# Kernel tuning notes

Hardware: AMD Instinct MI355X
Metric: run time of the kernel (lower is better)

The kernel has to match this reference:

```python
import jax, jax.numpy as jnp
import numpy as np


def setup_inputs() -> dict:
    key = jax.random.key(0)
    k1, k2, k3, k4, k5 = jax.random.split(key, 5)
    B, C, H, W = 8, 512, 64, 64
    mid = C // 8
    x = jax.random.normal(k1, (B, C, H, W), dtype=jnp.float32)
    # 1x1 convs (no bias) are just channel-mixing matrices
    Wb = jax.random.normal(k2, (mid, C), dtype=jnp.float32) * (1.0 / np.sqrt(C))
    Wc = jax.random.normal(k3, (mid, C), dtype=jnp.float32) * (1.0 / np.sqrt(C))
    Wd = jax.random.normal(k4, (C, C), dtype=jnp.float32) * (1.0 / np.sqrt(C))
    gamma = jax.random.normal(k5, (1,), dtype=jnp.float32)
    return {"x": x, "Wb": Wb, "Wc": Wc, "Wd": Wd, "gamma": gamma}


def reference(x, Wb, Wc, Wd, gamma):
    B, C, H, W = x.shape
    N = H * W
    xf = x.reshape(B, C, N)                          # (B, C, N)
    b = jnp.einsum('mc,bcn->bnm', Wb, xf)            # queries  (B, N, mid)
    c = jnp.einsum('mc,bcn->bmn', Wc, xf)            # keys     (B, mid, N)
    d = jnp.einsum('oc,bcn->bno', Wd, xf)            # values   (B, N, C)
    # unscaled scores, softmax over keys (last dim), as in the source
    attn = jax.nn.softmax(jnp.einsum('bnm,bmk->bnk', b, c), axis=-1)  # (B, N, N)
    out = jnp.einsum('bnk,bko->bno', attn, d)        # (B, N, C)
    out = out.transpose(0, 2, 1).reshape(B, C, H, W)
    return gamma * out + x
```

## Files before the change

kernel.cpp:

```cpp
#include <hip/hip_runtime.h>

typedef unsigned short u16;
typedef _Float16 f16x8 __attribute__((ext_vector_type(8)));
typedef short bf16x8 __attribute__((ext_vector_type(8)));
typedef float f32x16 __attribute__((ext_vector_type(16)));
typedef unsigned int u32x4 __attribute__((ext_vector_type(4)));
typedef unsigned int u32x2 __attribute__((ext_vector_type(2)));

#define LOG2E 1.44269504088896340736f

static __device__ __forceinline__ u16 f2h(float f){
  union { _Float16 h; u16 u; } v; v.h = (_Float16)f; return v.u;
}
static __device__ __forceinline__ u16 f2bf(float f){
  union { float f; unsigned u; } v; v.f = f;
  return (u16)((v.u + 0x7fffu + ((v.u >> 16) & 1u)) >> 16);
}
static __device__ __forceinline__ unsigned pk2bf(float lo, float hi){
  unsigned r; asm("v_cvt_pk_bf16_f32 %0, %1, %2" : "=v"(r) : "v"(lo), "v"(hi)); return r;
}
static __device__ __forceinline__ float ex2(float x){
#if __has_builtin(__builtin_amdgcn_exp2f)
  return __builtin_amdgcn_exp2f(x);
#else
  return exp2f(x);
#endif
}
#define PSWAP(a, b) asm("v_permlane32_swap_b32 %0, %1" : "+v"(a), "+v"(b))

__global__ __launch_bounds__(256) void k_tr(const float* __restrict__ x, u16* __restrict__ xt){
  int bx = blockIdx.x;
  int nb = bx & 63, cb = (bx >> 6) & 7, b = bx >> 9;
  __shared__ u16 lt[64 * 68];
  int t = threadIdx.x;
  int cl = t >> 4, n0 = (t & 15) * 4;
  const float* xp = x + ((size_t)(b * 512 + cb * 64)) * 4096 + nb * 64;
#pragma unroll
  for (int i = 0; i < 4; ++i) {
    int c = cl + i * 16;
    float4 v = *(const float4*)(xp + (size_t)c * 4096 + n0);
    u16* d = &lt[c * 68 + n0];
    d[0] = f2h(v.x); d[1] = f2h(v.y); d[2] = f2h(v.z); d[3] = f2h(v.w);
  }
  __syncthreads();
  u16* xo = xt + ((size_t)(b * 4096 + nb * 64)) * 512 + cb * 64;
#pragma unroll
  for (int i = 0; i < 2; ++i) {
    int s = t + i * 256;
    int n = s >> 3, ch = s & 7;
    u32x4 o;
#pragma unroll
    for (int j = 0; j < 4; ++j) {
      u16 a = lt[(ch * 8 + 2 * j) * 68 + n];
      u16 bb = lt[(ch * 8 + 2 * j + 1) * 68 + n];
      o[j] = (unsigned)a | ((unsigned)bb << 16);
    }
    *(u32x4*)(xo + (size_t)n * 512 + ch * 8) = o;
  }
}

__global__ __launch_bounds__(512) void k_pqk(const u16* __restrict__ xt, const float* __restrict__ wb,
                                             const float* __restrict__ wc, u16* __restrict__ qk){
  int bx = blockIdx.x;
  int nb = bx & 31, b = bx >> 5;
  __shared__ u16 lx[128 * 64];
  __shared__ u16 lw[128 * 64];
  int t = threadIdx.x, w = t >> 6, l = t & 63, hi = l >> 5, ln = l & 31;
  int wr = w >> 1, wcol = w & 1;
  f32x16 acc[2] = {};
  for (int kt = 0; kt < 8; ++kt) {
    int c0 = kt * 64;
#pragma unroll
    for (int i = 0; i < 2; ++i) {
      int s = t + i * 512; int row = s >> 3, ch = s & 7;
      u32x4 v = *(const u32x4*)(xt + ((size_t)(b * 4096 + nb * 128 + row)) * 512 + c0 + ch * 8);
      *(u32x4*)((char*)lx + ((row * 128 + ch * 16) ^ ((row & 7) << 4))) = v;
    }
#pragma unroll
    for (int i = 0; i < 4; ++i) {
      int s = t + i * 512; int row = s >> 4, c4 = s & 15;
      const float* src = (row < 64) ? (wb + (size_t)row * 512 + c0 + c4 * 4)
                                    : (wc + (size_t)(row - 64) * 512 + c0 + c4 * 4);
      float4 v = *(const float4*)src;
      float sc = (row < 64) ? LOG2E : 1.0f;
      unsigned lo = (unsigned)f2h(v.x * sc) | ((unsigned)f2h(v.y * sc) << 16);
      unsigned h2 = (unsigned)f2h(v.z * sc) | ((unsigned)f2h(v.w * sc) << 16);
      unsigned long long qv = ((unsigned long long)h2 << 32) | lo;
      *(unsigned long long*)((char*)lw + ((row * 128 + c4 * 8) ^ ((row & 7) << 4))) = qv;
    }
    __syncthreads();
#pragma unroll
    for (int cc = 0; cc < 4; ++cc) {
      int ra = wr * 32 + ln;
      f16x8 a = *(const f16x8*)((char*)lx + ((ra * 128 + cc * 32 + hi * 16) ^ ((ra & 7) << 4)));
#pragma unroll
      for (int mt = 0; mt < 2; ++mt) {
        int rb = wcol * 64 + mt * 32 + ln;
        f16x8 bb = *(const f16x8*)((char*)lw + ((rb * 128 + cc * 32 + hi * 16) ^ ((rb & 7) << 4)));
        acc[mt] = __builtin_amdgcn_mfma_f32_32x32x16_f16(a, bb, acc[mt], 0, 0, 0);
      }
    }
    __syncthreads();
  }
#pragma unroll
  for (int mt = 0; mt < 2; ++mt)
#pragma unroll
    for (int r = 0; r < 16; ++r) {
      int n = wr * 32 + (r & 3) + 8 * (r >> 2) + 4 * hi;
      int m = wcol * 64 + mt * 32 + ln;
      qk[((size_t)(b * 4096 + nb * 128 + n)) * 128 + m] = f2h(acc[mt][r]);
    }
}

__global__ __launch_bounds__(512) void k_pv(const u16* __restrict__ xt, const float* __restrict__ wd,
                                            u16* __restrict__ vt){
  int bx = blockIdx.x;
  int nb = bx & 31, ob = (bx >> 5) & 3, b = bx >> 7;
  __shared__ u16 lx[128 * 64];
  __shared__ u16 lw[128 * 64];
  int t = threadIdx.x, w = t >> 6, l = t & 63, hi = l >> 5, ln = l & 31;
  int wr = w >> 2, wn = w & 3;
  f32x16 acc[2] = {};
  for (int kt = 0; kt < 8; ++kt) {
    int c0 = kt * 64;
#pragma unroll
    for (int i = 0; i < 2; ++i) {
      int s = t + i * 512; int row = s >> 3, ch = s & 7;
      u32x4 v = *(const u32x4*)(xt + ((size_t)(b * 4096 + nb * 128 + row)) * 512 + c0 + ch * 8);
      *(u32x4*)((char*)lx + ((row * 128 + ch * 16) ^ ((row & 7) << 4))) = v;
    }
#pragma unroll
    for (int i = 0; i < 4; ++i) {
      int s = t + i * 512; int row = s >> 4, c4 = s & 15;
      const float* src = wd + (size_t)(ob * 128 + row) * 512 + c0 + c4 * 4;
      float4 v = *(const float4*)src;
      unsigned lo = (unsigned)f2h(v.x) | ((unsigned)f2h(v.y) << 16);
      unsigned h2 = (unsigned)f2h(v.z) | ((unsigned)f2h(v.w) << 16);
      unsigned long long qv = ((unsigned long long)h2 << 32) | lo;
      *(unsigned long long*)((char*)lw + ((row * 128 + c4 * 8) ^ ((row & 7) << 4))) = qv;
    }
    __syncthreads();
#pragma unroll
    for (int cc = 0; cc < 4; ++cc) {
      int rb = wn * 32 + ln;
      f16x8 bb = *(const f16x8*)((char*)lx + ((rb * 128 + cc * 32 + hi * 16) ^ ((rb & 7) << 4)));
#pragma unroll
      for (int ot = 0; ot < 2; ++ot) {
        int ra = wr * 64 + ot * 32 + ln;
        f16x8 a = *(const f16x8*)((char*)lw + ((ra * 128 + cc * 32 + hi * 16) ^ ((ra & 7) << 4)));
        acc[ot] = __builtin_amdgcn_mfma_f32_32x32x16_f16(a, bb, acc[ot], 0, 0, 0);
      }
    }
    __syncthreads();
  }
#pragma unroll
  for (int ot = 0; ot < 2; ++ot)
#pragma unroll
    for (int r = 0; r < 16; ++r) {
      int o = ob * 128 + wr * 64 + ot * 32 + (r & 3) + 8 * (r >> 2) + 4 * hi;
      int n = nb * 128 + wn * 32 + ln;
      vt[((size_t)(b * 512 + o)) * 4096 + n] = f2bf(acc[ot][r]);
    }
}

__global__ __launch_bounds__(512, 1) void k_attn2(const u16* __restrict__ qk, const u16* __restrict__ vt,
                                                  const float* __restrict__ x, const float* __restrict__ gamma,
                                                  float* __restrict__ out){
  __shared__ char smem[87040];
  int bx = blockIdx.x;
  int orig = (bx & 7) * 32 + (bx >> 3);
  int combo = orig >> 4, qt = orig & 15;
  int b = combo >> 1, oc2 = combo & 1;
  int obase = oc2 * 256;
  int t = threadIdx.x, w = t >> 6, l = t & 63, hi = l >> 5, ln = l & 31;
  int q = qt * 256 + w * 32 + ln;
  size_t b4096 = (size_t)b * 4096;
  f16x8 qf[4];
  {
    const u16* qrow = qk + (b4096 + q) * 128;
#pragma unroll
    for (int ch = 0; ch < 4; ++ch) qf[ch] = *(const f16x8*)(qrow + ch * 16 + hi * 8);
  }
  int rowS = t >> 3, chS = t & 7;
  unsigned w8 = (unsigned)(rowS * 17 + chS * 2);
  unsigned rb8[4];
#pragma unroll
  for (int cc = 0; cc < 4; ++cc)
    rb8[cc] = (unsigned)(ln * 17 + cc * 4 + hi * 2);
  const u16* gK = qk + (b4096 + rowS) * 128 + 64 + chS * 8;
  const u16* gV0 = vt + ((size_t)(b * 512 + obase + rowS)) * 4096 + chS * 8;
  const u16* gV1 = gV0 + (size_t)64 * 4096;
  const u16* gV2 = gV0 + (size_t)128 * 4096;
  const u16* gV3 = gV0 + (size_t)192 * 4096;
  u32x4 kreg = *(const u32x4*)gK;
  u32x4 vr0 = *(const u32x4*)gV0, vr1 = *(const u32x4*)gV1;
  u32x4 vr2 = *(const u32x4*)gV2, vr3 = *(const u32x4*)gV3;
  {
    char* bp = smem;
    *(u32x2*)(bp + w8 * 8)              = u32x2{kreg[0], kreg[1]};
    *(u32x2*)(bp + w8 * 8 + 8)          = u32x2{kreg[2], kreg[3]};
    *(u32x2*)(bp + 8704  + w8 * 8)      = u32x2{vr0[0], vr0[1]};
    *(u32x2*)(bp + 8704  + w8 * 8 + 8)  = u32x2{vr0[2], vr0[3]};
    *(u32x2*)(bp + 17408 + w8 * 8)      = u32x2{vr1[0], vr1[1]};
    *(u32x2*)(bp + 17408 + w8 * 8 + 8)  = u32x2{vr1[2], vr1[3]};
    *(u32x2*)(bp + 26112 + w8 * 8)      = u32x2{vr2[0], vr2[1]};
    *(u32x2*)(bp + 26112 + w8 * 8 + 8)  = u32x2{vr2[2], vr2[3]};
    *(u32x2*)(bp + 34816 + w8 * 8)      = u32x2{vr3[0], vr3[1]};
    *(u32x2*)(bp + 34816 + w8 * 8 + 8)  = u32x2{vr3[2], vr3[3]};
  }
  gK += 8192; gV0 += 64; gV1 += 64; gV2 += 64; gV3 += 64;
  f32x16 acc[8] = {};
  float lacc = 0.0f;
  for (int kt = 0; kt < 64; ++kt) {
    __syncthreads();
    char* bufp = smem + (kt & 1) * 43520;
    char* bufn = smem + ((kt + 1) & 1) * 43520;
    if (kt < 63) {
      kreg = *(const u32x4*)gK;
      vr0 = *(const u32x4*)gV0; vr1 = *(const u32x4*)gV1;
      vr2 = *(const u32x4*)gV2; vr3 = *(const u32x4*)gV3;
      gK += 8192; gV0 += 64; gV1 += 64; gV2 += 64; gV3 += 64;
    }
    f32x16 s0 = {}, s1 = {};
    __builtin_amdgcn_s_setprio(1);
#pragma unroll
    for (int cc = 0; cc < 4; ++cc) {
      union { u32x2 d[2]; f16x8 v; } k0, k1;
      const char* p0 = bufp + rb8[cc] * 8;
      const char* p1 = p0 + 4352;
      k0.d[0] = *(const u32x2*)p0;  k0.d[1] = *(const u32x2*)(p0 + 8);
      k1.d[0] = *(const u32x2*)p1;  k1.d[1] = *(const u32x2*)(p1 + 8);
      s0 = __builtin_amdgcn_mfma_f32_32x32x16_f16(k0.v, qf[cc], s0, 0, 0, 0);
      s1 = __builtin_amdgcn_mfma_f32_32x32x16_f16(k1.v, qf[cc], s1, 0, 0, 0);
    }
    __builtin_amdgcn_s_setprio(0);
#pragma unroll
    for (int r = 0; r < 16; ++r) s0[r] = ex2(s0[r]);
#pragma unroll
    for (int r = 0; r < 16; ++r) s1[r] = ex2(s1[r]);
    {
      float p[16];
#pragma unroll
      for (int r = 0; r < 16; ++r) p[r] = s0[r] + s1[r];
#pragma unroll
      for (int d = 8; d >= 1; d >>= 1)
#pragma unroll
        for (int r = 0; r < d; ++r) p[r] += p[r + d];
      lacc += p[0];
    }
    unsigned c0[8], c1[8];
#pragma unroll
    for (int i = 0; i < 8; ++i) c0[i] = pk2bf(s0[2 * i], s0[2 * i + 1]);
#pragma unroll
    for (int i = 0; i < 8; ++i) c1[i] = pk2bf(s1[2 * i], s1[2 * i + 1]);
    PSWAP(c0[0], c0[2]); PSWAP(c0[1], c0[3]); PSWAP(c0[4], c0[6]); PSWAP(c0[5], c0[7]);
    PSWAP(c1[0], c1[2]); PSWAP(c1[1], c1[3]); PSWAP(c1[4], c1[6]); PSWAP(c1[5], c1[7]);
    union U8 { unsigned u[4]; bf16x8 v; } pa[4];
#pragma unroll
    for (int j = 0; j < 4; ++j) { pa[0].u[j] = c0[j]; pa[1].u[j] = c0[4 + j]; pa[2].u[j] = c1[j]; pa[3].u[j] = c1[4 + j]; }
    __builtin_amdgcn_s_setprio(1);
#pragma unroll
    for (int kc = 0; kc < 4; ++kc) {
      const char* pv = bufp + 8704 + rb8[kc] * 8;
#pragma unroll
      for (int ot = 0; ot < 8; ++ot) {
        union { u32x2 d[2]; bf16x8 v; } vb;
        const char* p = pv + ot * 4352;
        vb.d[0] = *(const u32x2*)p;  vb.d[1] = *(const u32x2*)(p + 8);
        acc[ot] = __builtin_amdgcn_mfma_f32_32x32x16_bf16(pa[kc].v, vb.v, acc[ot], 0, 0, 0);
      }
    }
    __builtin_amdgcn_s_setprio(0);
    if (kt < 63) {
      *(u32x2*)(bufn + w8 * 8)              = u32x2{kreg[0], kreg[1]};
      *(u32x2*)(bufn + w8 * 8 + 8)          = u32x2{kreg[2], kreg[3]};
      *(u32x2*)(bufn + 8704  + w8 * 8)      = u32x2{vr0[0], vr0[1]};
      *(u32x2*)(bufn + 8704  + w8 * 8 + 8)  = u32x2{vr0[2], vr0[3]};
      *(u32x2*)(bufn + 17408 + w8 * 8)      = u32x2{vr1[0], vr1[1]};
      *(u32x2*)(bufn + 17408 + w8 * 8 + 8)  = u32x2{vr1[2], vr1[3]};
      *(u32x2*)(bufn + 26112 + w8 * 8)      = u32x2{vr2[0], vr2[1]};
      *(u32x2*)(bufn + 26112 + w8 * 8 + 8)  = u32x2{vr2[2], vr2[3]};
      *(u32x2*)(bufn + 34816 + w8 * 8)      = u32x2{vr3[0], vr3[1]};
      *(u32x2*)(bufn + 34816 + w8 * 8 + 8)  = u32x2{vr3[2], vr3[3]};
    }
  }
  float l_tot = lacc + __shfl_xor(lacc, 32);
  float sinv = gamma[0] / l_tot;
  __syncthreads();
  float* tb = (float*)smem + w * 1056;
#pragma unroll
  for (int ot = 0; ot < 8; ++ot) {
#pragma unroll
    for (int r = 0; r < 16; ++r) {
      int qr = (r & 3) + 8 * (r >> 2) + 4 * hi;
      tb[ln * 33 + qr] = acc[ot][r];
    }
#pragma unroll
    for (int it = 0; it < 16; ++it) {
      int orow = it * 2 + hi;
      float v = tb[orow * 33 + ln];
      size_t gi = (((size_t)(b * 512 + obase + ot * 32 + orow)) << 12) + (size_t)(qt * 256 + w * 32 + ln);
      out[gi] = sinv * v + x[gi];
    }
    __syncthreads();
  }
}

extern "C" void kernel_launch(void* const* d_in, const int* in_sizes, int n_in,
                              void* d_out, int out_size, void* d_ws, size_t ws_size,
                              hipStream_t stream) {
  (void)in_sizes; (void)n_in; (void)out_size; (void)ws_size;
  const float* x     = (const float*)d_in[0];
  const float* wb    = (const float*)d_in[1];
  const float* wc    = (const float*)d_in[2];
  const float* wd    = (const float*)d_in[3];
  const float* gamma = (const float*)d_in[4];
  float* out = (float*)d_out;
  char* ws = (char*)d_ws;
  u16* xt  = (u16*)ws;
  u16* qkb = (u16*)(ws + 33554432);
  u16* vtb = (u16*)(ws + 41943040);
  k_tr   <<<dim3(4096), dim3(256), 0, stream>>>(x, xt);
  k_pqk  <<<dim3(256),  dim3(512), 0, stream>>>(xt, wb, wc, qkb);
  k_pv   <<<dim3(1024), dim3(512), 0, stream>>>(xt, wd, vtb);
  k_attn2<<<dim3(256),  dim3(512), 0, stream>>>(qkb, vtb, x, gamma, out);
}
```

Measured before the change: 254.3 us.

## Fuse transpose and QKV projections into one kernel with pre-converted fp16 weights

Replaces the separate transpose, QK-projection and V-projection kernels with one fused kernel. It reads fp32 x directly, transposes it through shared memory, and computes all 640 output rows (V, Q, K) against each x tile. A small pre-pass converts the weights to fp16 once, which removes the per-block weight conversion and the round trip of the transposed xt buffer through global memory. In exchange the fused kernel launches only 256 blocks with large accumulators and heavy LDS use, so occupancy and parallelism are lower than in the old 1024-block V projection.

```diff
diff --git a/kernel.cpp b/kernel.cpp
--- a/kernel.cpp
+++ b/kernel.cpp
@@ -28,139 +28,129 @@
 }
 #define PSWAP(a, b) asm("v_permlane32_swap_b32 %0, %1" : "+v"(a), "+v"(b))
 
-__global__ __launch_bounds__(256) void k_tr(const float* __restrict__ x, u16* __restrict__ xt){
+__global__ __launch_bounds__(256) void k_wcvt(const float* __restrict__ wb, const float* __restrict__ wc,
+                                              const float* __restrict__ wd, u16* __restrict__ w16){
+  int row = blockIdx.x, t = threadIdx.x;
+  const float* src; float sc;
+  if (row < 512)      { src = wd + (size_t)row * 512;        sc = 1.0f;  }
+  else if (row < 576) { src = wb + (size_t)(row - 512) * 512; sc = LOG2E; }
+  else                { src = wc + (size_t)(row - 576) * 512; sc = 1.0f;  }
+  float2 v = *(const float2*)(src + t * 2);
+  unsigned pk = (unsigned)f2h(v.x * sc) | ((unsigned)f2h(v.y * sc) << 16);
+  *(unsigned*)(w16 + (size_t)row * 512 + t * 2) = pk;
+}
+
+__global__ __launch_bounds__(512, 1) void k_fused(const float* __restrict__ x, const u16* __restrict__ w16,
+                                                  u16* __restrict__ qkb, u16* __restrict__ vtb){
+  __shared__ u16 ltmp[64 * 140];
+  __shared__ u16 lx[128 * 68];
+  __shared__ u16 lw[640 * 68];
   int bx = blockIdx.x;
-  int nb = bx & 63, cb = (bx >> 6) & 7, b = bx >> 9;
-  __shared__ u16 lt[64 * 68];
-  int t = threadIdx.x;
-  int cl = t >> 4, n0 = (t & 15) * 4;
-  const float* xp = x + ((size_t)(b * 512 + cb * 64)) * 4096 + nb * 64;
-#pragma unroll
-  for (int i = 0; i < 4; ++i) {
-    int c = cl + i * 16;
-    float4 v = *(const float4*)(xp + (size_t)c * 4096 + n0);
-    u16* d = &lt[c * 68 + n0];
-    d[0] = f2h(v.x); d[1] = f2h(v.y); d[2] = f2h(v.z); d[3] = f2h(v.w);
-  }
-  __syncthreads();
-  u16* xo = xt + ((size_t)(b * 4096 + nb * 64)) * 512 + cb * 64;
-#pragma unroll
-  for (int i = 0; i < 2; ++i) {
-    int s = t + i * 256;
-    int n = s >> 3, ch = s & 7;
-    u32x4 o;
-#pragma unroll
-    for (int j = 0; j < 4; ++j) {
-      u16 a = lt[(ch * 8 + 2 * j) * 68 + n];
-      u16 bb = lt[(ch * 8 + 2 * j + 1) * 68 + n];
-      o[j] = (unsigned)a | ((unsigned)bb << 16);
-    }
-    *(u32x4*)(xo + (size_t)n * 512 + ch * 8) = o;
-  }
-}
-
-__global__ __launch_bounds__(512) void k_pqk(const u16* __restrict__ xt, const float* __restrict__ wb,
-                                             const float* __restrict__ wc, u16* __restrict__ qk){
-  int bx = blockIdx.x;
-  int nb = bx & 31, b = bx >> 5;
-  __shared__ u16 lx[128 * 64];
-  __shared__ u16 lw[128 * 64];
+  int b = bx >> 5, nb = bx & 31;
   int t = threadIdx.x, w = t >> 6, l = t & 63, hi = l >> 5, ln = l & 31;
-  int wr = w >> 1, wcol = w & 1;
-  f32x16 acc[2] = {};
+  int i = w & 1, j = w >> 1;
+  size_t b4096 = (size_t)b * 4096;
+  f32x16 acc[5][2] = {};
+  int cS = t >> 3, ncS = t & 7;
+  int nT = t & 127, q4 = t >> 7;
   for (int kt = 0; kt < 8; ++kt) {
     int c0 = kt * 64;
-#pragma unroll
-    for (int i = 0; i < 2; ++i) {
-      int s = t + i * 512; int row = s >> 3, ch = s & 7;
-      u32x4 v = *(const u32x4*)(xt + ((size_t)(b * 4096 + nb * 128 + row)) * 512 + c0 + ch * 8);
-      *(u32x4*)((char*)lx + ((row * 128 + ch * 16) ^ ((row & 7) << 4))) = v;
-    }
-#pragma unroll
-    for (int i = 0; i < 4; ++i) {
-      int s = t + i * 512; int row = s >> 4, c4 = s & 15;
-      const float* src = (row < 64) ? (wb + (size_t)row * 512 + c0 + c4 * 4)
-                                    : (wc + (size_t)(row - 64) * 512 + c0 + c4 * 4);
-      float4 v = *(const float4*)src;
-      float sc = (row < 64) ? LOG2E : 1.0f;
-      unsigned lo = (unsigned)f2h(v.x * sc) | ((unsigned)f2h(v.y * sc) << 16);
-      unsigned h2 = (unsigned)f2h(v.z * sc) | ((unsigned)f2h(v.w * sc) << 16);
-      unsigned long long qv = ((unsigned long long)h2 << 32) | lo;
-      *(unsigned long long*)((char*)lw + ((row * 128 + c4 * 8) ^ ((row & 7) << 4))) = qv;
+    {
+      const float* xp = x + ((size_t)(b * 512 + c0 + cS)) * 4096 + nb * 128 + ncS * 16;
+      u16* d = &ltmp[cS * 140 + ncS * 16];
+#pragma unroll
+      for (int g = 0; g < 4; ++g) {
+        float4 v = *(const float4*)(xp + g * 4);
+        unsigned lo = (unsigned)f2h(v.x) | ((unsigned)f2h(v.y) << 16);
+        unsigned h2 = (unsigned)f2h(v.z) | ((unsigned)f2h(v.w) << 16);
+        *(u32x2*)(d + g * 4) = u32x2{lo, h2};
+      }
+    }
+#pragma unroll
+    for (int k10 = 0; k10 < 10; ++k10) {
+      int slot = t + 512 * k10;
+      int row = slot >> 3, ch8 = slot & 7;
+      u32x4 wv = *(const u32x4*)(w16 + (size_t)row * 512 + c0 + ch8 * 8);
+      u16* d = &lw[row * 68 + ch8 * 8];
+      *(u32x2*)d       = u32x2{wv[0], wv[1]};
+      *(u32x2*)(d + 4) = u32x2{wv[2], wv[3]};
+    }
+    __syncthreads();
+    {
+      u16 tmp[16];
+#pragma unroll
+      for (int k = 0; k < 16; ++k) tmp[k] = ltmp[(q4 * 16 + k) * 140 + nT];
+      u16* d = &lx[nT * 68 + q4 * 16];
+#pragma unroll
+      for (int g = 0; g < 4; ++g) {
+        unsigned lo = (unsigned)tmp[g * 4]     | ((unsigned)tmp[g * 4 + 1] << 16);
+        unsigned h2 = (unsigned)tmp[g * 4 + 2] | ((unsigned)tmp[g * 4 + 3] << 16);
+        *(u32x2*)(d + g * 4) = u32x2{lo, h2};
+      }
     }
     __syncthreads();
 #pragma unroll
     for (int cc = 0; cc < 4; ++cc) {
-      int ra = wr * 32 + ln;
-      f16x8 a = *(const f16x8*)((char*)lx + ((ra * 128 + cc * 32 + hi * 16) ^ ((ra & 7) << 4)));
-#pragma unroll
-      for (int mt = 0; mt < 2; ++mt) {
-        int rb = wcol * 64 + mt * 32 + ln;
-        f16x8 bb = *(const f16x8*)((char*)lw + ((rb * 128 + cc * 32 + hi * 16) ^ ((rb & 7) << 4)));
-        acc[mt] = __builtin_amdgcn_mfma_f32_32x32x16_f16(a, bb, acc[mt], 0, 0, 0);
-      }
-    }
-    __syncthreads();
-  }
-#pragma unroll
-  for (int mt = 0; mt < 2; ++mt)
-#pragma unroll
-    for (int r = 0; r < 16; ++r) {
-      int n = wr * 32 + (r & 3) + 8 * (r >> 2) + 4 * hi;
-      int m = wcol * 64 + mt * 32 + ln;
-      qk[((size_t)(b * 4096 + nb * 128 + n)) * 128 + m] = f2h(acc[mt][r]);
-    }
-}
-
-__global__ __launch_bounds__(512) void k_pv(const u16* __restrict__ xt, const float* __restrict__ wd,
-                                            u16* __restrict__ vt){
-  int bx = blockIdx.x;
-  int nb = bx & 31, ob = (bx >> 5) & 3, b = bx >> 7;
-  __shared__ u16 lx[128 * 64];
-  __shared__ u16 lw[128 * 64];
-  int t = threadIdx.x, w = t >> 6, l = t & 63, hi = l >> 5, ln = l & 31;
-  int wr = w >> 2, wn = w & 3;
-  f32x16 acc[2] = {};
-  for (int kt = 0; kt < 8; ++kt) {
-    int c0 = kt * 64;
-#pragma unroll
-    for (int i = 0; i < 2; ++i) {
-      int s = t + i * 512; int row = s >> 3, ch = s & 7;
-      u32x4 v = *(const u32x4*)(xt + ((size_t)(b * 4096 + nb * 128 + row)) * 512 + c0 + ch * 8);
-      *(u32x4*)((char*)lx + ((row * 128 + ch * 16) ^ ((row & 7) << 4))) = v;
-    }
-#pragma unroll
-    for (int i = 0; i < 4; ++i) {
-      int s = t + i * 512; int row = s >> 4, c4 = s & 15;
-      const float* src = wd + (size_t)(ob * 128 + row) * 512 + c0 + c4 * 4;
-      float4 v = *(const float4*)src;
-      unsigned lo = (unsigned)f2h(v.x) | ((unsigned)f2h(v.y) << 16);
-      unsigned h2 = (unsigned)f2h(v.z) | ((unsigned)f2h(v.w) << 16);
-      unsigned long long qv = ((unsigned long long)h2 << 32) | lo;
-      *(unsigned long long*)((char*)lw + ((row * 128 + c4 * 8) ^ ((row & 7) << 4))) = qv;
-    }
-    __syncthreads();
-#pragma unroll
-    for (int cc = 0; cc < 4; ++cc) {
-      int rb = wn * 32 + ln;
-      f16x8 bb = *(const f16x8*)((char*)lx + ((rb * 128 + cc * 32 + hi * 16) ^ ((rb & 7) << 4)));
-#pragma unroll
-      for (int ot = 0; ot < 2; ++ot) {
-        int ra = wr * 64 + ot * 32 + ln;
-        f16x8 a = *(const f16x8*)((char*)lw + ((ra * 128 + cc * 32 + hi * 16) ^ ((ra & 7) << 4)));
-        acc[ot] = __builtin_amdgcn_mfma_f32_32x32x16_f16(a, bb, acc[ot], 0, 0, 0);
-      }
-    }
-    __syncthreads();
-  }
-#pragma unroll
-  for (int ot = 0; ot < 2; ++ot)
-#pragma unroll
-    for (int r = 0; r < 16; ++r) {
-      int o = ob * 128 + wr * 64 + ot * 32 + (r & 3) + 8 * (r >> 2) + 4 * hi;
-      int n = nb * 128 + wn * 32 + ln;
-      vt[((size_t)(b * 512 + o)) * 4096 + n] = f2bf(acc[ot][r]);
-    }
+      union { u32x2 d[2]; f16x8 v; } bf[2];
+#pragma unroll
+      for (int u = 0; u < 2; ++u) {
+        const u16* p = &lx[(i * 64 + u * 32 + ln) * 68 + cc * 16 + hi * 8];
+        bf[u].d[0] = *(const u32x2*)p; bf[u].d[1] = *(const u32x2*)(p + 4);
+      }
+#pragma unroll
+      for (int s = 0; s < 5; ++s) {
+        union { u32x2 d[2]; f16x8 v; } af;
+        const u16* p = &lw[(j * 160 + s * 32 + ln) * 68 + cc * 16 + hi * 8];
+        af.d[0] = *(const u32x2*)p; af.d[1] = *(const u32x2*)(p + 4);
+#pragma unroll
+        for (int u = 0; u < 2; ++u)
+          acc[s][u] = __builtin_amdgcn_mfma_f32_32x32x16_f16(af.v, bf[u].v, acc[s][u], 0, 0, 0);
+      }
+    }
+    __syncthreads();
+  }
+#pragma unroll
+  for (int s = 0; s < 5; ++s) {
+    int rt = j * 160 + s * 32;
+    if (rt < 512) {
+#pragma unroll
+      for (int u = 0; u < 2; ++u) {
+        int n = nb * 128 + i * 64 + u * 32 + ln;
+#pragma unroll
+        for (int r = 0; r < 16; ++r) {
+          int o = rt + (r & 3) + 8 * (r >> 2) + 4 * hi;
+          vtb[((size_t)(b * 512 + o)) * 4096 + n] = f2bf(acc[s][u][r]);
+        }
+      }
+    }
+  }
+  u16* qkl = lw;
+  if (j == 3) {
+#pragma unroll
+    for (int s = 1; s < 5; ++s) {
+      int mbase = (s - 1) * 32;
+#pragma unroll
+      for (int u = 0; u < 2; ++u) {
+        int nl = i * 64 + u * 32 + ln;
+#pragma unroll
+        for (int r = 0; r < 16; ++r) {
+          int m = mbase + (r & 3) + 8 * (r >> 2) + 4 * hi;
+          qkl[nl * 132 + m] = f2h(acc[s][u][r]);
+        }
+      }
+    }
+  }
+  __syncthreads();
+  {
+    int n2 = t >> 2, ch = t & 3;
+    u16* dst = qkb + (b4096 + nb * 128 + n2) * 128 + ch * 32;
+#pragma unroll
+    for (int g = 0; g < 4; ++g) {
+      u32x2 d0 = *(const u32x2*)(&qkl[n2 * 132 + ch * 32 + g * 8]);
+      u32x2 d1 = *(const u32x2*)(&qkl[n2 * 132 + ch * 32 + g * 8 + 4]);
+      *(u32x4*)(dst + g * 8) = u32x4{d0[0], d0[1], d1[0], d1[1]};
+    }
+  }
 }
 
 __global__ __launch_bounds__(512, 1) void k_attn2(const u16* __restrict__ qk, const u16* __restrict__ vt,
@@ -250,14 +240,14 @@
     }
     unsigned c0[8], c1[8];
 #pragma unroll
-    for (int i = 0; i < 8; ++i) c0[i] = pk2bf(s0[2 * i], s0[2 * i + 1]);
-#pragma unroll
-    for (int i = 0; i < 8; ++i) c1[i] = pk2bf(s1[2 * i], s1[2 * i + 1]);
+    for (int ii = 0; ii < 8; ++ii) c0[ii] = pk2bf(s0[2 * ii], s0[2 * ii + 1]);
+#pragma unroll
+    for (int ii = 0; ii < 8; ++ii) c1[ii] = pk2bf(s1[2 * ii], s1[2 * ii + 1]);
     PSWAP(c0[0], c0[2]); PSWAP(c0[1], c0[3]); PSWAP(c0[4], c0[6]); PSWAP(c0[5], c0[7]);
     PSWAP(c1[0], c1[2]); PSWAP(c1[1], c1[3]); PSWAP(c1[4], c1[6]); PSWAP(c1[5], c1[7]);
     union U8 { unsigned u[4]; bf16x8 v; } pa[4];
 #pragma unroll
-    for (int j = 0; j < 4; ++j) { pa[0].u[j] = c0[j]; pa[1].u[j] = c0[4 + j]; pa[2].u[j] = c1[j]; pa[3].u[j] = c1[4 + j]; }
+    for (int jj = 0; jj < 4; ++jj) { pa[0].u[jj] = c0[jj]; pa[1].u[jj] = c0[4 + jj]; pa[2].u[jj] = c1[jj]; pa[3].u[jj] = c1[4 + jj]; }
     __builtin_amdgcn_s_setprio(1);
 #pragma unroll
     for (int kc = 0; kc < 4; ++kc) {
@@ -317,11 +307,10 @@
   const float* gamma = (const float*)d_in[4];
   float* out = (float*)d_out;
   char* ws = (char*)d_ws;
-  u16* xt  = (u16*)ws;
-  u16* qkb = (u16*)(ws + 33554432);
-  u16* vtb = (u16*)(ws + 41943040);
-  k_tr   <<<dim3(4096), dim3(256), 0, stream>>>(x, xt);
-  k_pqk  <<<dim3(256),  dim3(512), 0, stream>>>(xt, wb, wc, qkb);
-  k_pv   <<<dim3(1024), dim3(512), 0, stream>>>(xt, wd, vtb);
-  k_attn2<<<dim3(256),  dim3(512), 0, stream>>>(qkb, vtb, x, gamma, out);
-}
+  u16* w16 = (u16*)ws;
+  u16* qkb = (u16*)(ws + 1048576);
+  u16* vtb = (u16*)(ws + 9437184);
+  k_wcvt <<<dim3(640), dim3(256), 0, stream>>>(wb, wc, wd, w16);
+  k_fused<<<dim3(256), dim3(512), 0, stream>>>(x, w16, qkb, vtb);
+  k_attn2<<<dim3(256), dim3(512), 0, stream>>>(qkb, vtb, x, gamma, out);
+}
```

New measurement: 237.1 us. 1.07x faster.
